# Performance work log

Measured on AMD Instinct MI355X. Metric: run time of the kernel, lower is better.

Reference implementation:

```python
import jax, jax.numpy as jnp
import numpy as np

B, S, D_IN, D_OUT = 4, 4096, 1024, 1024

def setup_inputs() -> dict:
    key = jax.random.key(0)
    kx, kq, kk, kv = jax.random.split(key, 4)
    scale = 1.0 / np.sqrt(D_IN)
    return {
        "x": jax.random.normal(kx, (B, S, D_IN), dtype=jnp.float32),
        "Wq": jax.random.normal(kq, (D_IN, D_OUT), dtype=jnp.float32) * scale,
        "Wk": jax.random.normal(kk, (D_IN, D_OUT), dtype=jnp.float32) * scale,
        "Wv": jax.random.normal(kv, (D_IN, D_OUT), dtype=jnp.float32) * scale,
    }

def reference(x, Wq, Wk, Wv):
    # x: [B, S, d_in]; W*: [d_in, d_out]
    B_, S_, _ = x.shape
    d_out = Wq.shape[1]
    q = jnp.einsum("bsi,io->bso", x, Wq)
    k = jnp.einsum("bsi,io->bso", x, Wk)
    v = jnp.einsum("bsi,io->bso", x, Wv)
    # scores: [B, S, S]
    scores = jnp.einsum("bqo,bko->bqk", q, k)
    # causal mask: position q attends to k <= q (intended semantics of the
    # tril-buffer masked_fill); masked entries -> -inf before softmax.
    causal = jnp.tril(jnp.ones((S_, S_), dtype=bool))  # True where allowed
    scores = jnp.where(causal[None, :, :], scores, -jnp.inf)
    attn = jax.nn.softmax(scores / jnp.sqrt(jnp.asarray(d_out, scores.dtype)), axis=-1)
    # dropout p=0.0 -> identity
    return jnp.einsum("bqk,bko->bqo", attn, v)
```

## Files before the change

### kernel.cpp

```cpp
#include <hip/hip_runtime.h>


typedef __attribute__((ext_vector_type(8))) short bh8;
typedef __attribute__((ext_vector_type(4))) float f32x4;
typedef __attribute__((ext_vector_type(4))) unsigned int u32x4;
typedef __attribute__((ext_vector_type(2))) unsigned int u32x2;

#define BATCH 4
#define SEQ   4096
#define DIM   1024
#define MTOT  (BATCH * SEQ)

__device__ __forceinline__ unsigned short f2bf(float f) {
  union { float f; unsigned int u; } v; v.f = f;
  return (unsigned short)((v.u + 0x7FFFu + ((v.u >> 16) & 1u)) >> 16);
}

__device__ __forceinline__ void gload_lds16(const void* g, void* l) {
  __builtin_amdgcn_global_load_lds(
      (const __attribute__((address_space(1))) unsigned int*)g,
      (__attribute__((address_space(3))) unsigned int*)l, 16, 0, 0);
}

__global__ __launch_bounds__(256)
void k_convert_x(const float* __restrict__ x, unsigned short* __restrict__ xb) {
  size_t idx = ((size_t)blockIdx.x * 256 + threadIdx.x) * 8;
  f32x4 v0 = *(const f32x4*)(x + idx);
  f32x4 v1 = *(const f32x4*)(x + idx + 4);
  u32x4 pk;
  pk[0] = (unsigned)f2bf(v0[0]) | ((unsigned)f2bf(v0[1]) << 16);
  pk[1] = (unsigned)f2bf(v0[2]) | ((unsigned)f2bf(v0[3]) << 16);
  pk[2] = (unsigned)f2bf(v1[0]) | ((unsigned)f2bf(v1[1]) << 16);
  pk[3] = (unsigned)f2bf(v1[2]) | ((unsigned)f2bf(v1[3]) << 16);
  *(u32x4*)(xb + idx) = pk;
}

__global__ __launch_bounds__(256)
void k_transpose_w(const float* __restrict__ Wq, const float* __restrict__ Wk,
                   const float* __restrict__ Wv, unsigned short* __restrict__ wt) {
  __shared__ float tile[32][33];
  const int z = blockIdx.z;
  const float* W = (z == 0) ? Wq : ((z == 1) ? Wk : Wv);
  unsigned short* out = wt + (size_t)z * DIM * DIM;
  const int tx = threadIdx.x, ty = threadIdx.y;
  const int n = blockIdx.x * 32 + tx;
  const int k = blockIdx.y * 32 + ty;
#pragma unroll
  for (int i = 0; i < 32; i += 8)
    tile[ty + i][tx] = W[(size_t)(k + i) * DIM + n];
  __syncthreads();
  const int k2 = blockIdx.y * 32 + tx;
  const int n2 = blockIdx.x * 32 + ty;
#pragma unroll
  for (int i = 0; i < 32; i += 8)
    out[(size_t)(n2 + i) * DIM + k2] = f2bf(tile[tx][ty + i]);
}

__global__ __launch_bounds__(256)
void k_qkv_gemm(const unsigned short* __restrict__ xb, const unsigned short* __restrict__ wt,
                unsigned short* __restrict__ qb, unsigned short* __restrict__ kb,
                unsigned short* __restrict__ vt) {
  const int tid = threadIdx.x;
  const int l = tid & 63, w = tid >> 6;
  const int lane16 = l & 15, quad = l >> 4;
  const int wm = w & 1, wn = w >> 1;
  const int m0 = blockIdx.x * 128, n0 = blockIdx.y * 128, z = blockIdx.z;
  const unsigned short* wtz = wt + (size_t)z * DIM * DIM;

  __shared__ unsigned short As[128][32];
  __shared__ unsigned short Bs[128][32];

  const int lrow = l >> 2;
  const int lcol = (l & 3) * 8;

  f32x4 acc[4][4];
#pragma unroll
  for (int i = 0; i < 4; ++i)
#pragma unroll
    for (int j = 0; j < 4; ++j) acc[i][j] = (f32x4){0.f, 0.f, 0.f, 0.f};

  for (int k0 = 0; k0 < DIM; k0 += 32) {
#pragma unroll
    for (int i = 0; i < 2; ++i) {
      const int rbase = i * 64 + w * 16;
      const int row = rbase + lrow;
      gload_lds16(xb  + (size_t)(m0 + row) * DIM + k0 + lcol, &As[rbase][0]);
      gload_lds16(wtz + (size_t)(n0 + row) * DIM + k0 + lcol, &Bs[rbase][0]);
    }
    __syncthreads();
    bh8 a[4], b[4];
#pragma unroll
    for (int mt = 0; mt < 4; ++mt) a[mt] = *(const bh8*)&As[wm * 64 + mt * 16 + lane16][quad * 8];
#pragma unroll
    for (int nt = 0; nt < 4; ++nt) b[nt] = *(const bh8*)&Bs[wn * 64 + nt * 16 + lane16][quad * 8];
#pragma unroll
    for (int mt = 0; mt < 4; ++mt)
#pragma unroll
      for (int nt = 0; nt < 4; ++nt)
        acc[mt][nt] = __builtin_amdgcn_mfma_f32_16x16x32_bf16(a[mt], b[nt], acc[mt][nt], 0, 0, 0);
    __syncthreads();
  }

  if (z < 2) {
    unsigned short* outp = (z == 0) ? qb : kb;
#pragma unroll
    for (int mt = 0; mt < 4; ++mt)
#pragma unroll
      for (int nt = 0; nt < 4; ++nt) {
        int row = m0 + wm * 64 + mt * 16 + quad * 4;
        int col = n0 + wn * 64 + nt * 16 + lane16;
#pragma unroll
        for (int r = 0; r < 4; ++r)
          outp[(size_t)(row + r) * DIM + col] = f2bf(acc[mt][nt][r]);
      }
  } else {
#pragma unroll
    for (int mt = 0; mt < 4; ++mt)
#pragma unroll
      for (int nt = 0; nt < 4; ++nt) {
        int m = m0 + wm * 64 + mt * 16 + quad * 4;
        int bb = m >> 12, s = m & (SEQ - 1);
        int col = n0 + wn * 64 + nt * 16 + lane16;
        unsigned long long pk =
            (unsigned long long)f2bf(acc[mt][nt][0]) |
            ((unsigned long long)f2bf(acc[mt][nt][1]) << 16) |
            ((unsigned long long)f2bf(acc[mt][nt][2]) << 32) |
            ((unsigned long long)f2bf(acc[mt][nt][3]) << 48);
        *(unsigned long long*)(vt + (size_t)bb * DIM * SEQ + (size_t)col * SEQ + s) = pk;
      }
  }
}

__global__ __launch_bounds__(512, 2)
void k_attn(const unsigned short* __restrict__ qb, const unsigned short* __restrict__ kb,
            const unsigned short* __restrict__ vt, float* __restrict__ out) {
  const int tid = threadIdx.x;
  const int w = tid >> 6;
  const int l = tid & 63;
  const int lane16 = l & 15, quad = l >> 4;
  const int id = blockIdx.x;
  const int batch = id & 3;
  const int t = 127 - (id >> 2);
  const int q0 = t * 32;

  __shared__ float Pp[8][32][68];
  __shared__ unsigned short Psh[32][72];
  __shared__ float row_m[32], row_l[32], row_alpha[32];

  const size_t bbase = (size_t)batch * SEQ;
  const unsigned short* vtb = vt + (size_t)batch * DIM * SEQ;
  const float cexp = 0.04508422002778f;

  bh8 qf[2][4];
#pragma unroll
  for (int mt = 0; mt < 2; ++mt)
#pragma unroll
    for (int c = 0; c < 4; ++c)
      qf[mt][c] = *(const bh8*)(qb + (bbase + q0 + mt * 16 + lane16) * DIM +
                                w * 128 + c * 32 + quad * 8);

  f32x4 o[2][8];
#pragma unroll
  for (int mt = 0; mt < 2; ++mt)
#pragma unroll
    for (int nt = 0; nt < 8; ++nt) o[mt][nt] = (f32x4){0.f, 0.f, 0.f, 0.f};

  const int nk = (q0 + 95) >> 6;

  bh8 kf[4][4];
#pragma unroll
  for (int kt = 0; kt < 4; ++kt)
#pragma unroll
    for (int c = 0; c < 4; ++c)
      kf[kt][c] = *(const bh8*)(kb + (bbase + kt * 16 + lane16) * DIM +
                                w * 128 + c * 32 + quad * 8);

  for (int it = 0; it < nk; ++it) {
    const int k0 = it * 64;

    bh8 vfa[4][2];
#pragma unroll
    for (int nt = 0; nt < 4; ++nt)
#pragma unroll
      for (int kc = 0; kc < 2; ++kc)
        vfa[nt][kc] = *(const bh8*)(vtb + (size_t)(w * 128 + nt * 16 + lane16) * SEQ +
                                    k0 + kc * 32 + quad * 8);

    if (it == 0 && tid < 32) { row_m[tid] = -3.0e38f; row_l[tid] = 0.f; }

#pragma unroll
    for (int kt = 0; kt < 4; ++kt) {
      if (k0 + kt * 16 <= q0 + 31) {
#pragma unroll
        for (int mt = 0; mt < 2; ++mt) {
          f32x4 s = (f32x4){0.f, 0.f, 0.f, 0.f};
#pragma unroll
          for (int c = 0; c < 4; ++c)
            s = __builtin_amdgcn_mfma_f32_16x16x32_bf16(qf[mt][c], kf[kt][c], s, 0, 0, 0);
          int row = mt * 16 + quad * 4;
          int col = kt * 16 + lane16;
#pragma unroll
          for (int r = 0; r < 4; ++r)
            Pp[w][row + r][col] = s[r];
        }
      }
    }

    if (it + 1 < nk) {
#pragma unroll
      for (int kt = 0; kt < 4; ++kt)
#pragma unroll
        for (int c = 0; c < 4; ++c)
          kf[kt][c] = *(const bh8*)(kb + (bbase + k0 + 64 + kt * 16 + lane16) * DIM +
                                    w * 128 + c * 32 + quad * 8);
    }
    __syncthreads();

    {
      int r = tid >> 4, c0 = (tid & 15) * 4;
      int q = q0 + r;
      f32x4 sv = *(const f32x4*)&Pp[0][r][c0];
#pragma unroll
      for (int ww = 1; ww < 8; ++ww)
        sv += *(const f32x4*)&Pp[ww][r][c0];
#pragma unroll
      for (int j = 0; j < 4; ++j)
        if (k0 + c0 + j > q) sv[j] = -3.0e38f;
      float mx = fmaxf(fmaxf(sv[0], sv[1]), fmaxf(sv[2], sv[3]));
#pragma unroll
      for (int off = 1; off < 16; off <<= 1)
        mx = fmaxf(mx, __shfl_xor(mx, off));
      float mold = row_m[r];
      float mnew = fmaxf(mold, mx);
      float p0 = __builtin_amdgcn_exp2f((sv[0] - mnew) * cexp);
      float p1 = __builtin_amdgcn_exp2f((sv[1] - mnew) * cexp);
      float p2 = __builtin_amdgcn_exp2f((sv[2] - mnew) * cexp);
      float p3 = __builtin_amdgcn_exp2f((sv[3] - mnew) * cexp);
      float sum = (p0 + p1) + (p2 + p3);
#pragma unroll
      for (int off = 1; off < 16; off <<= 1)
        sum += __shfl_xor(sum, off);
      float alpha = __builtin_amdgcn_exp2f((mold - mnew) * cexp);
      u32x2 pk;
      pk[0] = (unsigned)f2bf(p0) | ((unsigned)f2bf(p1) << 16);
      pk[1] = (unsigned)f2bf(p2) | ((unsigned)f2bf(p3) << 16);
      *(u32x2*)&Psh[r][c0] = pk;
      if ((tid & 15) == 0) {
        row_m[r] = mnew;
        row_l[r] = alpha * row_l[r] + sum;
        row_alpha[r] = alpha;
      }
    }
    __syncthreads();

    {
      bh8 vfb[4][2];
#pragma unroll
      for (int nt = 0; nt < 4; ++nt)
#pragma unroll
        for (int kc = 0; kc < 2; ++kc)
          vfb[nt][kc] = *(const bh8*)(vtb + (size_t)(w * 128 + (nt + 4) * 16 + lane16) * SEQ +
                                      k0 + kc * 32 + quad * 8);

#pragma unroll
      for (int mt = 0; mt < 2; ++mt) {
        f32x4 al;
#pragma unroll
        for (int r = 0; r < 4; ++r) al[r] = row_alpha[mt * 16 + quad * 4 + r];
#pragma unroll
        for (int nt = 0; nt < 8; ++nt) o[mt][nt] *= al;
      }
      bh8 pf[2][2];
#pragma unroll
      for (int mt = 0; mt < 2; ++mt)
#pragma unroll
        for (int kc = 0; kc < 2; ++kc)
          pf[mt][kc] = *(const bh8*)&Psh[mt * 16 + lane16][kc * 32 + quad * 8];
#pragma unroll
      for (int kc = 0; kc < 2; ++kc) {
        if (k0 + kc * 32 <= q0 + 31) {
#pragma unroll
          for (int nt = 0; nt < 4; ++nt)
#pragma unroll
            for (int mt = 0; mt < 2; ++mt)
              o[mt][nt] = __builtin_amdgcn_mfma_f32_16x16x32_bf16(pf[mt][kc], vfa[nt][kc], o[mt][nt], 0, 0, 0);
#pragma unroll
          for (int nt = 0; nt < 4; ++nt)
#pragma unroll
            for (int mt = 0; mt < 2; ++mt)
              o[mt][nt + 4] = __builtin_amdgcn_mfma_f32_16x16x32_bf16(pf[mt][kc], vfb[nt][kc], o[mt][nt + 4], 0, 0, 0);
        }
      }
    }
  }

#pragma unroll
  for (int mt = 0; mt < 2; ++mt) {
    int row = mt * 16 + quad * 4;
    float il[4];
#pragma unroll
    for (int r = 0; r < 4; ++r) il[r] = 1.0f / row_l[row + r];
#pragma unroll
    for (int nt = 0; nt < 8; ++nt) {
      size_t base = (bbase + q0 + row) * DIM + w * 128 + nt * 16 + lane16;
#pragma unroll
      for (int r = 0; r < 4; ++r)
        out[base + (size_t)r * DIM] = o[mt][nt][r] * il[r];
    }
  }
}

extern "C" void kernel_launch(void* const* d_in, const int* in_sizes, int n_in,
                              void* d_out, int out_size, void* d_ws, size_t ws_size,
                              hipStream_t stream) {
  const float* x  = (const float*)d_in[0];
  const float* Wq = (const float*)d_in[1];
  const float* Wk = (const float*)d_in[2];
  const float* Wv = (const float*)d_in[3];
  float* out = (float*)d_out;

  char* ws = (char*)d_ws;
  const size_t XB_BYTES = (size_t)MTOT * DIM * 2;
  const size_t WT_BYTES = (size_t)3 * DIM * DIM * 2;
  unsigned short* xb = (unsigned short*)(ws);
  unsigned short* wt = (unsigned short*)(ws + XB_BYTES);
  unsigned short* qb = (unsigned short*)(ws + XB_BYTES + WT_BYTES);
  unsigned short* kb = qb + (size_t)MTOT * DIM;
  unsigned short* vt = kb + (size_t)MTOT * DIM;

  k_convert_x<<<dim3((MTOT * DIM) / (256 * 8)), dim3(256), 0, stream>>>(x, xb);
  k_transpose_w<<<dim3(32, 32, 3), dim3(32, 8), 0, stream>>>(Wq, Wk, Wv, wt);
  k_qkv_gemm<<<dim3(MTOT / 128, DIM / 128, 3), dim3(256), 0, stream>>>(xb, wt, qb, kb, vt);
  k_attn<<<dim3(512), dim3(512), 0, stream>>>(qb, kb, vt, out);
}
```

Baseline: 841.5 us.

## Restructure attention: split QK^T by key tile across waves, pipeline softmax/PV

Reworks the attention kernel so each wave computes a full-depth 16-key slice of QK^T using Q staged in swizzled shared memory, instead of the old scheme where each wave did a partial 128-dim product that had to be summed across 8 waves in LDS. Key blocks grow to 128, and score computation for block i is software-pipelined with softmax and PV for block i-1 through double-buffered score tiles, cutting to one barrier per iteration. Running max and sum now live in registers and are spread with shuffles. The cost is a larger LDS footprint (64KB Q plus scores), occupancy lowered to one block per CU, and K/V still read directly from global memory.

```diff
diff --git a/kernel.cpp b/kernel.cpp
--- a/kernel.cpp
+++ b/kernel.cpp
@@ -4,7 +4,6 @@
 typedef __attribute__((ext_vector_type(8))) short bh8;
 typedef __attribute__((ext_vector_type(4))) float f32x4;
 typedef __attribute__((ext_vector_type(4))) unsigned int u32x4;
-typedef __attribute__((ext_vector_type(2))) unsigned int u32x2;
 
 #define BATCH 4
 #define SEQ   4096
@@ -131,7 +130,7 @@
   }
 }
 
-__global__ __launch_bounds__(512, 2)
+__global__ __launch_bounds__(512, 1)
 void k_attn(const unsigned short* __restrict__ qb, const unsigned short* __restrict__ kb,
             const unsigned short* __restrict__ vt, float* __restrict__ out) {
   const int tid = threadIdx.x;
@@ -143,169 +142,156 @@
   const int t = 127 - (id >> 2);
   const int q0 = t * 32;
 
-  __shared__ float Pp[8][32][68];
-  __shared__ unsigned short Psh[32][72];
-  __shared__ float row_m[32], row_l[32], row_alpha[32];
+  __shared__ unsigned char Qs[32 * 2048];
+  __shared__ float Ps[2][32][140];
 
   const size_t bbase = (size_t)batch * SEQ;
   const unsigned short* vtb = vt + (size_t)batch * DIM * SEQ;
   const float cexp = 0.04508422002778f;
 
-  bh8 qf[2][4];
+  {
+    int row = tid >> 4;
+    const unsigned short* src = qb + (bbase + q0 + row) * DIM;
+#pragma unroll
+    for (int i = 0; i < 8; ++i) {
+      int cb = ((tid & 15) + i * 16) * 16;
+      bh8 v = *(const bh8*)(src + cb / 2);
+      *(bh8*)(Qs + row * 2048 + (cb ^ ((row & 7) << 4))) = v;
+    }
+  }
+
+  f32x4 o[2][8];
 #pragma unroll
   for (int mt = 0; mt < 2; ++mt)
 #pragma unroll
-    for (int c = 0; c < 4; ++c)
-      qf[mt][c] = *(const bh8*)(qb + (bbase + q0 + mt * 16 + lane16) * DIM +
-                                w * 128 + c * 32 + quad * 8);
-
-  f32x4 o[2][8];
-#pragma unroll
-  for (int mt = 0; mt < 2; ++mt)
-#pragma unroll
     for (int nt = 0; nt < 8; ++nt) o[mt][nt] = (f32x4){0.f, 0.f, 0.f, 0.f};
-
-  const int nk = (q0 + 95) >> 6;
-
-  bh8 kf[4][4];
-#pragma unroll
-  for (int kt = 0; kt < 4; ++kt)
-#pragma unroll
-    for (int c = 0; c < 4; ++c)
-      kf[kt][c] = *(const bh8*)(kb + (bbase + kt * 16 + lane16) * DIM +
-                                w * 128 + c * 32 + quad * 8);
-
-  for (int it = 0; it < nk; ++it) {
-    const int k0 = it * 64;
-
-    bh8 vfa[4][2];
-#pragma unroll
-    for (int nt = 0; nt < 4; ++nt)
-#pragma unroll
-      for (int kc = 0; kc < 2; ++kc)
-        vfa[nt][kc] = *(const bh8*)(vtb + (size_t)(w * 128 + nt * 16 + lane16) * SEQ +
-                                    k0 + kc * 32 + quad * 8);
-
-    if (it == 0 && tid < 32) { row_m[tid] = -3.0e38f; row_l[tid] = 0.f; }
-
-#pragma unroll
-    for (int kt = 0; kt < 4; ++kt) {
-      if (k0 + kt * 16 <= q0 + 31) {
-#pragma unroll
-        for (int mt = 0; mt < 2; ++mt) {
-          f32x4 s = (f32x4){0.f, 0.f, 0.f, 0.f};
-#pragma unroll
-          for (int c = 0; c < 4; ++c)
-            s = __builtin_amdgcn_mfma_f32_16x16x32_bf16(qf[mt][c], kf[kt][c], s, 0, 0, 0);
-          int row = mt * 16 + quad * 4;
-          int col = kt * 16 + lane16;
-#pragma unroll
-          for (int r = 0; r < 4; ++r)
-            Pp[w][row + r][col] = s[r];
-        }
-      }
-    }
-
-    if (it + 1 < nk) {
-#pragma unroll
-      for (int kt = 0; kt < 4; ++kt)
-#pragma unroll
-        for (int c = 0; c < 4; ++c)
-          kf[kt][c] = *(const bh8*)(kb + (bbase + k0 + 64 + kt * 16 + lane16) * DIM +
-                                    w * 128 + c * 32 + quad * 8);
+  float m_run[2] = {-3.0e38f, -3.0e38f};
+  float l_run[2] = {0.f, 0.f};
+
+  const int nk = (q0 + 32 + 127) >> 7;
+
+  __syncthreads();
+
+  for (int i = 0; i <= nk; ++i) {
+    if (i < nk) {
+      const int k0 = i << 7;
+      if (k0 + w * 16 <= q0 + 31) {
+        const unsigned short* kp = kb + (bbase + k0 + w * 16 + lane16) * DIM + quad * 8;
+        const unsigned char* qp0 = Qs + lane16 * 2048;
+        const unsigned char* qp1 = Qs + (16 + lane16) * 2048;
+        const int swz = (lane16 & 7) << 4;
+        f32x4 a0 = (f32x4){0.f, 0.f, 0.f, 0.f};
+        f32x4 a1 = (f32x4){0.f, 0.f, 0.f, 0.f};
+#pragma unroll 8
+        for (int cc = 0; cc < 32; ++cc) {
+          bh8 kf  = *(const bh8*)(kp + cc * 32);
+          bh8 qf0 = *(const bh8*)(qp0 + ((cc * 64 + quad * 16) ^ swz));
+          bh8 qf1 = *(const bh8*)(qp1 + ((cc * 64 + quad * 16) ^ swz));
+          a0 = __builtin_amdgcn_mfma_f32_16x16x32_bf16(qf0, kf, a0, 0, 0, 0);
+          a1 = __builtin_amdgcn_mfma_f32_16x16x32_bf16(qf1, kf, a1, 0, 0, 0);
+        }
+        float* pc = &Ps[i & 1][quad * 4][w * 16 + lane16];
+#pragma unroll
+        for (int r = 0; r < 4; ++r) {
+          pc[r * 140] = a0[r];
+          pc[(16 + r) * 140] = a1[r];
+        }
+      }
+    }
+
+    if (i >= 1) {
+      const int k0p = (i - 1) << 7;
+      const float* pb = &Ps[(i + 1) & 1][0][0];
+      bh8 pf[2][4];
+#pragma unroll
+      for (int mt = 0; mt < 2; ++mt) {
+        const int row = mt * 16 + lane16;
+        const int q = q0 + row;
+        const float* pr = pb + row * 140 + quad * 8;
+        f32x4 sv[8];
+#pragma unroll
+        for (int kc = 0; kc < 4; ++kc) {
+          sv[kc * 2]     = *(const f32x4*)(pr + kc * 32);
+          sv[kc * 2 + 1] = *(const f32x4*)(pr + kc * 32 + 4);
+        }
+#pragma unroll
+        for (int kc = 0; kc < 4; ++kc) {
+          int cb = k0p + kc * 32 + quad * 8;
+#pragma unroll
+          for (int jj = 0; jj < 4; ++jj) {
+            if (cb + jj > q)     sv[kc * 2][jj]     = -3.0e38f;
+            if (cb + 4 + jj > q) sv[kc * 2 + 1][jj] = -3.0e38f;
+          }
+        }
+        f32x4 m4 = sv[0];
+#pragma unroll
+        for (int u = 1; u < 8; ++u)
+#pragma unroll
+          for (int jj = 0; jj < 4; ++jj) m4[jj] = fmaxf(m4[jj], sv[u][jj]);
+        float mx = fmaxf(fmaxf(m4[0], m4[1]), fmaxf(m4[2], m4[3]));
+        mx = fmaxf(mx, __shfl_xor(mx, 16));
+        mx = fmaxf(mx, __shfl_xor(mx, 32));
+        float mold = m_run[mt];
+        float mnew = fmaxf(mold, mx);
+        float al = __builtin_amdgcn_exp2f((mold - mnew) * cexp);
+        f32x4 alr;
+#pragma unroll
+        for (int r = 0; r < 4; ++r)
+          alr[r] = __shfl(al, (quad << 4) | (quad * 4 + r));
+#pragma unroll
+        for (int nt = 0; nt < 8; ++nt) o[mt][nt] *= alr;
+        float rs = 0.f;
+#pragma unroll
+        for (int kc = 0; kc < 4; ++kc) {
+          union { bh8 v; unsigned short u[8]; } pk;
+#pragma unroll
+          for (int hh = 0; hh < 2; ++hh)
+#pragma unroll
+            for (int jj = 0; jj < 4; ++jj) {
+              float p = __builtin_amdgcn_exp2f((sv[kc * 2 + hh][jj] - mnew) * cexp);
+              rs += p;
+              pk.u[hh * 4 + jj] = f2bf(p);
+            }
+          pf[mt][kc] = pk.v;
+        }
+        rs += __shfl_xor(rs, 16);
+        rs += __shfl_xor(rs, 32);
+        l_run[mt] = l_run[mt] * al + rs;
+        m_run[mt] = mnew;
+      }
+#pragma unroll
+      for (int kc = 0; kc < 4; ++kc) {
+        if (k0p + kc * 32 <= q0 + 31) {
+          bh8 vf[8];
+#pragma unroll
+          for (int nt = 0; nt < 8; ++nt)
+            vf[nt] = *(const bh8*)(vtb + (size_t)(w * 128 + nt * 16 + lane16) * SEQ +
+                                   k0p + kc * 32 + quad * 8);
+#pragma unroll
+          for (int nt = 0; nt < 8; ++nt) {
+            o[0][nt] = __builtin_amdgcn_mfma_f32_16x16x32_bf16(pf[0][kc], vf[nt], o[0][nt], 0, 0, 0);
+            o[1][nt] = __builtin_amdgcn_mfma_f32_16x16x32_bf16(pf[1][kc], vf[nt], o[1][nt], 0, 0, 0);
+          }
+        }
+      }
     }
     __syncthreads();
-
-    {
-      int r = tid >> 4, c0 = (tid & 15) * 4;
-      int q = q0 + r;
-      f32x4 sv = *(const f32x4*)&Pp[0][r][c0];
-#pragma unroll
-      for (int ww = 1; ww < 8; ++ww)
-        sv += *(const f32x4*)&Pp[ww][r][c0];
-#pragma unroll
-      for (int j = 0; j < 4; ++j)
-        if (k0 + c0 + j > q) sv[j] = -3.0e38f;
-      float mx = fmaxf(fmaxf(sv[0], sv[1]), fmaxf(sv[2], sv[3]));
-#pragma unroll
-      for (int off = 1; off < 16; off <<= 1)
-        mx = fmaxf(mx, __shfl_xor(mx, off));
-      float mold = row_m[r];
-      float mnew = fmaxf(mold, mx);
-      float p0 = __builtin_amdgcn_exp2f((sv[0] - mnew) * cexp);
-      float p1 = __builtin_amdgcn_exp2f((sv[1] - mnew) * cexp);
-      float p2 = __builtin_amdgcn_exp2f((sv[2] - mnew) * cexp);
-      float p3 = __builtin_amdgcn_exp2f((sv[3] - mnew) * cexp);
-      float sum = (p0 + p1) + (p2 + p3);
-#pragma unroll
-      for (int off = 1; off < 16; off <<= 1)
-        sum += __shfl_xor(sum, off);
-      float alpha = __builtin_amdgcn_exp2f((mold - mnew) * cexp);
-      u32x2 pk;
-      pk[0] = (unsigned)f2bf(p0) | ((unsigned)f2bf(p1) << 16);
-      pk[1] = (unsigned)f2bf(p2) | ((unsigned)f2bf(p3) << 16);
-      *(u32x2*)&Psh[r][c0] = pk;
-      if ((tid & 15) == 0) {
-        row_m[r] = mnew;
-        row_l[r] = alpha * row_l[r] + sum;
-        row_alpha[r] = alpha;
-      }
-    }
-    __syncthreads();
-
-    {
-      bh8 vfb[4][2];
-#pragma unroll
-      for (int nt = 0; nt < 4; ++nt)
-#pragma unroll
-        for (int kc = 0; kc < 2; ++kc)
-          vfb[nt][kc] = *(const bh8*)(vtb + (size_t)(w * 128 + (nt + 4) * 16 + lane16) * SEQ +
-                                      k0 + kc * 32 + quad * 8);
-
-#pragma unroll
-      for (int mt = 0; mt < 2; ++mt) {
-        f32x4 al;
-#pragma unroll
-        for (int r = 0; r < 4; ++r) al[r] = row_alpha[mt * 16 + quad * 4 + r];
-#pragma unroll
-        for (int nt = 0; nt < 8; ++nt) o[mt][nt] *= al;
-      }
-      bh8 pf[2][2];
-#pragma unroll
-      for (int mt = 0; mt < 2; ++mt)
-#pragma unroll
-        for (int kc = 0; kc < 2; ++kc)
-          pf[mt][kc] = *(const bh8*)&Psh[mt * 16 + lane16][kc * 32 + quad * 8];
-#pragma unroll
-      for (int kc = 0; kc < 2; ++kc) {
-        if (k0 + kc * 32 <= q0 + 31) {
-#pragma unroll
-          for (int nt = 0; nt < 4; ++nt)
-#pragma unroll
-            for (int mt = 0; mt < 2; ++mt)
-              o[mt][nt] = __builtin_amdgcn_mfma_f32_16x16x32_bf16(pf[mt][kc], vfa[nt][kc], o[mt][nt], 0, 0, 0);
-#pragma unroll
-          for (int nt = 0; nt < 4; ++nt)
-#pragma unroll
-            for (int mt = 0; mt < 2; ++mt)
-              o[mt][nt + 4] = __builtin_amdgcn_mfma_f32_16x16x32_bf16(pf[mt][kc], vfb[nt][kc], o[mt][nt + 4], 0, 0, 0);
-        }
-      }
-    }
   }
 
 #pragma unroll
   for (int mt = 0; mt < 2; ++mt) {
+    float il = 1.0f / l_run[mt];
+    f32x4 ilr;
+#pragma unroll
+    for (int r = 0; r < 4; ++r)
+      ilr[r] = __shfl(il, (quad << 4) | (quad * 4 + r));
     int row = mt * 16 + quad * 4;
-    float il[4];
-#pragma unroll
-    for (int r = 0; r < 4; ++r) il[r] = 1.0f / row_l[row + r];
 #pragma unroll
     for (int nt = 0; nt < 8; ++nt) {
       size_t base = (bbase + q0 + row) * DIM + w * 128 + nt * 16 + lane16;
 #pragma unroll
       for (int r = 0; r < 4; ++r)
-        out[base + (size_t)r * DIM] = o[mt][nt][r] * il[r];
+        out[base + (size_t)r * DIM] = o[mt][nt][r] * ilr[r];
     }
   }
 }
```

Result: faster. 775.1 us (-7.9%).
